# Kernel tuning notes

Hardware: AMD Instinct MI355X
Metric: run time of the kernel (lower is better)

## Reference

```python
import jax, jax.numpy as jnp
import numpy as np

N_NODES = 100000
N_EDGES = 600000
D_IN = 128
D_OUT = 512  # hidden_size * gates_num = 128 * 4


def setup_inputs() -> dict:
    key = jax.random.key(0)
    k1, k2, k3, k4 = jax.random.split(key, 4)
    x = jax.random.normal(k1, (N_NODES, D_IN), dtype=jnp.float32)
    edge_index = jax.random.randint(k2, (2, N_EDGES), 0, N_NODES, dtype=jnp.int64)
    W = jax.random.normal(k3, (D_OUT, D_IN), dtype=jnp.float32) * (1.0 / np.sqrt(D_IN))
    b = jax.random.normal(k4, (D_OUT,), dtype=jnp.float32) * 0.01
    return {"x": x, "edge_index": edge_index, "W": W, "b": b}


def reference(x, edge_index, W, b):
    row, col = edge_index[0], edge_index[1]
    # gather neighbor features and scatter-add into destination nodes
    agg = jax.ops.segment_sum(x[col], row, num_segments=x.shape[0])  # [N, D_IN]
    out = x + agg  # residual
    return out @ W.T + b  # [N, D_OUT]
```

## Files before the change

### kernel.cpp

```cpp
#include <hip/hip_runtime.h>
#include <hip/hip_bf16.h>

#define N_NODES 100000
#define N_EDGES 600000
#define D_IN 128
#define D_OUT 512
#define CAP 40
#define OVF_CAP 1024

typedef __bf16 bf16x8 __attribute__((ext_vector_type(8)));
typedef __bf16 bf16x2 __attribute__((ext_vector_type(2)));
typedef float f32x4 __attribute__((ext_vector_type(4)));

#define OFF_CNT   25600000
#define OFF_OVFC  26000000
#define OFF_OVF   26000016
#define OFF_BUCK  26008208

__global__ void k_bucket(const int* __restrict__ ei, int* __restrict__ cnt,
                         int* __restrict__ bucket, int* __restrict__ ovf_cnt,
                         int2* __restrict__ ovf) {
    int e = blockIdx.x * blockDim.x + threadIdx.x;
    if (e >= N_EDGES) return;
    int r = ei[e];
    int c = ei[N_EDGES + e];
    int slot = atomicAdd(&cnt[r], 1);
    if (slot < CAP) {
        bucket[(size_t)r * CAP + slot] = c;
    } else {
        int oi = atomicAdd(ovf_cnt, 1);
        if (oi < OVF_CAP) ovf[oi] = make_int2(r, c);
    }
}

__global__ void k_agg(const float* __restrict__ x, const int* __restrict__ cnt,
                      const int* __restrict__ bucket, const int* __restrict__ ovf_cnt,
                      const int2* __restrict__ ovf, __bf16* __restrict__ h) {
    int gw = (blockIdx.x * blockDim.x + threadIdx.x) >> 6;
    if (gw >= N_NODES) return;
    int lane = threadIdx.x & 63;
    const float2* xr = (const float2*)x;

    float2 acc = xr[(size_t)gw * 64 + lane];
    float ax2 = 0.f, ay2 = 0.f;

    int deg = __builtin_amdgcn_readfirstlane(cnt[gw]);
    int dmin = deg < CAP ? deg : CAP;
    const int* bk = bucket + (size_t)gw * CAP;

    int d = 0;
    for (; d + 1 < dmin; d += 2) {
        int c0 = __builtin_amdgcn_readfirstlane(bk[d]);
        int c1 = __builtin_amdgcn_readfirstlane(bk[d + 1]);
        float2 v0 = xr[(size_t)c0 * 64 + lane];
        float2 v1 = xr[(size_t)c1 * 64 + lane];
        acc.x += v0.x; acc.y += v0.y;
        ax2 += v1.x;   ay2 += v1.y;
    }
    if (d < dmin) {
        int c0 = __builtin_amdgcn_readfirstlane(bk[d]);
        float2 v0 = xr[(size_t)c0 * 64 + lane];
        acc.x += v0.x; acc.y += v0.y;
    }
    acc.x += ax2; acc.y += ay2;

    if (deg > CAP) {
        int n = *ovf_cnt;
        if (n > OVF_CAP) n = OVF_CAP;
        for (int i = 0; i < n; ++i) {
            int2 e = ovf[i];
            if (e.x == gw) {
                float2 v = xr[(size_t)e.y * 64 + lane];
                acc.x += v.x; acc.y += v.y;
            }
        }
    }

    bf16x2 o = { (__bf16)acc.x, (__bf16)acc.y };
    ((bf16x2*)h)[(size_t)gw * 64 + lane] = o;
}

#define BM 128
#define BN 64
#define LDA 136
#define LDB 136

__device__ inline bf16x8 cvt8(float4 v0, float4 v1) {
    bf16x8 u = { (__bf16)v0.x, (__bf16)v0.y, (__bf16)v0.z, (__bf16)v0.w,
                 (__bf16)v1.x, (__bf16)v1.y, (__bf16)v1.z, (__bf16)v1.w };
    return u;
}

__launch_bounds__(256, 2)
__global__ void k_gemm(const __bf16* __restrict__ h, const float* __restrict__ W,
                       const float* __restrict__ bias, float* __restrict__ out) {
    __shared__ __bf16 As[BM * LDA];
    __shared__ __bf16 Bs[BN * LDB];

    int tid = threadIdx.x;
    int m0 = blockIdx.y * BM;
    int n0 = blockIdx.x * BN;

    #pragma unroll
    for (int it = 0; it < 8; ++it) {
        int i = tid + it * 256;
        int r = i >> 4;
        int c = (i & 15) << 3;
        int gr = m0 + r;
        if (gr > N_NODES - 1) gr = N_NODES - 1;
        *(bf16x8*)&As[r * LDA + c] = *(const bf16x8*)(h + (size_t)gr * D_IN + c);
    }
    #pragma unroll
    for (int it = 0; it < 4; ++it) {
        int i = tid + it * 256;
        int r = i >> 4;
        int c = (i & 15) << 3;
        const float* src = W + (size_t)(n0 + r) * D_IN + c;
        float4 v0 = *(const float4*)(src);
        float4 v1 = *(const float4*)(src + 4);
        *(bf16x8*)&Bs[r * LDB + c] = cvt8(v0, v1);
    }
    __syncthreads();

    int lane = tid & 63;
    int wave = tid >> 6;
    int wm = wave & 1;
    int wn = wave >> 1;
    int quad = lane >> 4;
    int l16 = lane & 15;

    f32x4 acc[4][2] = {};

    const __bf16* Abase = &As[(wm * 64 + l16) * LDA + quad * 8];
    const __bf16* Bbase = &Bs[(wn * 32 + l16) * LDB + quad * 8];

    #pragma unroll
    for (int ks = 0; ks < 4; ++ks) {
        bf16x8 a0 = *(const bf16x8*)(Abase + ks * 32);
        bf16x8 a1 = *(const bf16x8*)(Abase + 16 * LDA + ks * 32);
        bf16x8 a2 = *(const bf16x8*)(Abase + 32 * LDA + ks * 32);
        bf16x8 a3 = *(const bf16x8*)(Abase + 48 * LDA + ks * 32);
        bf16x8 b0 = *(const bf16x8*)(Bbase + ks * 32);
        bf16x8 b1 = *(const bf16x8*)(Bbase + 16 * LDB + ks * 32);
        acc[0][0] = __builtin_amdgcn_mfma_f32_16x16x32_bf16(a0, b0, acc[0][0], 0, 0, 0);
        acc[0][1] = __builtin_amdgcn_mfma_f32_16x16x32_bf16(a0, b1, acc[0][1], 0, 0, 0);
        acc[1][0] = __builtin_amdgcn_mfma_f32_16x16x32_bf16(a1, b0, acc[1][0], 0, 0, 0);
        acc[1][1] = __builtin_amdgcn_mfma_f32_16x16x32_bf16(a1, b1, acc[1][1], 0, 0, 0);
        acc[2][0] = __builtin_amdgcn_mfma_f32_16x16x32_bf16(a2, b0, acc[2][0], 0, 0, 0);
        acc[2][1] = __builtin_amdgcn_mfma_f32_16x16x32_bf16(a2, b1, acc[2][1], 0, 0, 0);
        acc[3][0] = __builtin_amdgcn_mfma_f32_16x16x32_bf16(a3, b0, acc[3][0], 0, 0, 0);
        acc[3][1] = __builtin_amdgcn_mfma_f32_16x16x32_bf16(a3, b1, acc[3][1], 0, 0, 0);
    }

    float bias0 = bias[n0 + wn * 32 + l16];
    float bias1 = bias[n0 + wn * 32 + 16 + l16];
    #pragma unroll
    for (int mt = 0; mt < 4; ++mt) {
        int mrow = m0 + wm * 64 + mt * 16 + quad * 4;
        #pragma unroll
        for (int nt = 0; nt < 2; ++nt) {
            int ncol = n0 + wn * 32 + nt * 16 + l16;
            float bv = nt ? bias1 : bias0;
            #pragma unroll
            for (int rg = 0; rg < 4; ++rg) {
                int m = mrow + rg;
                if (m < N_NODES)
                    out[(size_t)m * D_OUT + ncol] = acc[mt][nt][rg] + bv;
            }
        }
    }
}

extern "C" void kernel_launch(void* const* d_in, const int* in_sizes, int n_in,
                              void* d_out, int out_size, void* d_ws, size_t ws_size,
                              hipStream_t stream) {
    const float* x  = (const float*)d_in[0];
    const int*   ei = (const int*)d_in[1];
    const float* W  = (const float*)d_in[2];
    const float* b  = (const float*)d_in[3];
    float* out = (float*)d_out;

    char* ws = (char*)d_ws;
    __bf16* h    = (__bf16*)ws;
    int* cnt     = (int*)(ws + OFF_CNT);
    int* ovf_cnt = (int*)(ws + OFF_OVFC);
    int2* ovf    = (int2*)(ws + OFF_OVF);
    int* bucket  = (int*)(ws + OFF_BUCK);

    hipMemsetAsync(cnt, 0, (OFF_OVFC - OFF_CNT) + 16, stream);

    k_bucket<<<(N_EDGES + 255) / 256, 256, 0, stream>>>(ei, cnt, bucket, ovf_cnt, ovf);
    k_agg<<<(N_NODES * 64 + 255) / 256, 256, 0, stream>>>(x, cnt, bucket, ovf_cnt, ovf, h);
    k_gemm<<<dim3(D_OUT / BN, (N_NODES + BM - 1) / BM), 256, 0, stream>>>(h, W, b, out);
}
```

Before: 389.7 us.

## Make GEMM persistent with register-resident W fragments and prefetched A strips

The GEMM becomes a persistent kernel: each wave holds a 128-column slice of W as bf16 MFMA fragments in registers and loops over 16-row strips of h. It loads the next strip directly from global memory while computing the current one, and drops shared memory and the block barrier. This removes the repeated per-block reloading and conversion of W and the LDS staging. The cost is heavy register use (128 VGPRs for the B fragments), which may limit occupancy under the 256-thread, 2-block launch bound, and only 512 concurrent waves stream the 100k-row output.

Result: slower. 403.7 us (+3.6%).

```diff
diff --git a/kernel.cpp b/kernel.cpp
--- a/kernel.cpp
+++ b/kernel.cpp
@@ -80,10 +80,9 @@
     ((bf16x2*)h)[(size_t)gw * 64 + lane] = o;
 }
 
-#define BM 128
-#define BN 64
-#define LDA 136
-#define LDB 136
+#define N_STRIPS 6250
+#define WAVE_SLOTS 512
+#define GEMM_ITERS 13
 
 __device__ inline bf16x8 cvt8(float4 v0, float4 v1) {
     bf16x8 u = { (__bf16)v0.x, (__bf16)v0.y, (__bf16)v0.z, (__bf16)v0.w,
@@ -94,80 +93,67 @@
 __launch_bounds__(256, 2)
 __global__ void k_gemm(const __bf16* __restrict__ h, const float* __restrict__ W,
                        const float* __restrict__ bias, float* __restrict__ out) {
-    __shared__ __bf16 As[BM * LDA];
-    __shared__ __bf16 Bs[BN * LDB];
-
     int tid = threadIdx.x;
-    int m0 = blockIdx.y * BM;
-    int n0 = blockIdx.x * BN;
-
-    #pragma unroll
-    for (int it = 0; it < 8; ++it) {
-        int i = tid + it * 256;
-        int r = i >> 4;
-        int c = (i & 15) << 3;
-        int gr = m0 + r;
-        if (gr > N_NODES - 1) gr = N_NODES - 1;
-        *(bf16x8*)&As[r * LDA + c] = *(const bf16x8*)(h + (size_t)gr * D_IN + c);
-    }
-    #pragma unroll
-    for (int it = 0; it < 4; ++it) {
-        int i = tid + it * 256;
-        int r = i >> 4;
-        int c = (i & 15) << 3;
-        const float* src = W + (size_t)(n0 + r) * D_IN + c;
-        float4 v0 = *(const float4*)(src);
-        float4 v1 = *(const float4*)(src + 4);
-        *(bf16x8*)&Bs[r * LDB + c] = cvt8(v0, v1);
-    }
-    __syncthreads();
-
     int lane = tid & 63;
     int wave = tid >> 6;
-    int wm = wave & 1;
-    int wn = wave >> 1;
-    int quad = lane >> 4;
-    int l16 = lane & 15;
+    int nq = blockIdx.x;
+    int q = lane >> 4;
+    int n16 = lane & 15;
 
-    f32x4 acc[4][2] = {};
+    bf16x8 bfrag[8][4];
+    {
+        const float* wb = W + (size_t)(nq * 128 + n16) * D_IN + q * 8;
+        #pragma unroll
+        for (int nt = 0; nt < 8; ++nt)
+            #pragma unroll
+            for (int ks = 0; ks < 4; ++ks) {
+                const float* src = wb + (size_t)nt * 16 * D_IN + ks * 32;
+                float4 v0 = *(const float4*)(src);
+                float4 v1 = *(const float4*)(src + 4);
+                bfrag[nt][ks] = cvt8(v0, v1);
+            }
+    }
+    float biasr[8];
+    #pragma unroll
+    for (int nt = 0; nt < 8; ++nt)
+        biasr[nt] = bias[nq * 128 + nt * 16 + n16];
 
-    const __bf16* Abase = &As[(wm * 64 + l16) * LDA + quad * 8];
-    const __bf16* Bbase = &Bs[(wn * 32 + l16) * LDB + quad * 8];
+    int g = blockIdx.y * 4 + wave;
 
-    #pragma unroll
-    for (int ks = 0; ks < 4; ++ks) {
-        bf16x8 a0 = *(const bf16x8*)(Abase + ks * 32);
-        bf16x8 a1 = *(const bf16x8*)(Abase + 16 * LDA + ks * 32);
-        bf16x8 a2 = *(const bf16x8*)(Abase + 32 * LDA + ks * 32);
-        bf16x8 a3 = *(const bf16x8*)(Abase + 48 * LDA + ks * 32);
-        bf16x8 b0 = *(const bf16x8*)(Bbase + ks * 32);
-        bf16x8 b1 = *(const bf16x8*)(Bbase + 16 * LDB + ks * 32);
-        acc[0][0] = __builtin_amdgcn_mfma_f32_16x16x32_bf16(a0, b0, acc[0][0], 0, 0, 0);
-        acc[0][1] = __builtin_amdgcn_mfma_f32_16x16x32_bf16(a0, b1, acc[0][1], 0, 0, 0);
-        acc[1][0] = __builtin_amdgcn_mfma_f32_16x16x32_bf16(a1, b0, acc[1][0], 0, 0, 0);
-        acc[1][1] = __builtin_amdgcn_mfma_f32_16x16x32_bf16(a1, b1, acc[1][1], 0, 0, 0);
-        acc[2][0] = __builtin_amdgcn_mfma_f32_16x16x32_bf16(a2, b0, acc[2][0], 0, 0, 0);
-        acc[2][1] = __builtin_amdgcn_mfma_f32_16x16x32_bf16(a2, b1, acc[2][1], 0, 0, 0);
-        acc[3][0] = __builtin_amdgcn_mfma_f32_16x16x32_bf16(a3, b0, acc[3][0], 0, 0, 0);
-        acc[3][1] = __builtin_amdgcn_mfma_f32_16x16x32_bf16(a3, b1, acc[3][1], 0, 0, 0);
+    bf16x8 af[4];
+    if (g < N_STRIPS) {
+        const __bf16* ab = h + (size_t)(g * 16 + n16) * D_IN + q * 8;
+        #pragma unroll
+        for (int ks = 0; ks < 4; ++ks) af[ks] = *(const bf16x8*)(ab + ks * 32);
     }
 
-    float bias0 = bias[n0 + wn * 32 + l16];
-    float bias1 = bias[n0 + wn * 32 + 16 + l16];
-    #pragma unroll
-    for (int mt = 0; mt < 4; ++mt) {
-        int mrow = m0 + wm * 64 + mt * 16 + quad * 4;
-        #pragma unroll
-        for (int nt = 0; nt < 2; ++nt) {
-            int ncol = n0 + wn * 32 + nt * 16 + l16;
-            float bv = nt ? bias1 : bias0;
+    for (int it = 0; it < GEMM_ITERS; ++it) {
+        int gn = g + WAVE_SLOTS;
+        bf16x8 afn[4];
+        if (it + 1 < GEMM_ITERS && gn < N_STRIPS) {
+            const __bf16* ab = h + (size_t)(gn * 16 + n16) * D_IN + q * 8;
             #pragma unroll
-            for (int rg = 0; rg < 4; ++rg) {
-                int m = mrow + rg;
-                if (m < N_NODES)
-                    out[(size_t)m * D_OUT + ncol] = acc[mt][nt][rg] + bv;
+            for (int ks = 0; ks < 4; ++ks) afn[ks] = *(const bf16x8*)(ab + ks * 32);
+        }
+        if (g < N_STRIPS) {
+            f32x4 acc[8] = {};
+            #pragma unroll
+            for (int ks = 0; ks < 4; ++ks)
+                #pragma unroll
+                for (int nt = 0; nt < 8; ++nt)
+                    acc[nt] = __builtin_amdgcn_mfma_f32_16x16x32_bf16(
+                        af[ks], bfrag[nt][ks], acc[nt], 0, 0, 0);
+            float* ob = out + (size_t)(g * 16 + q * 4) * D_OUT + nq * 128 + n16;
+            #pragma unroll
+            for (int nt = 0; nt < 8; ++nt) {
+                #pragma unroll
+                for (int rg = 0; rg < 4; ++rg)
+                    ob[(size_t)rg * D_OUT + nt * 16] = acc[nt][rg] + biasr[nt];
             }
         }
+        g = gn;
+        #pragma unroll
+        for (int ks = 0; ks < 4; ++ks) af[ks] = afn[ks];
     }
 }
 
@@ -191,5 +177,5 @@
 
     k_bucket<<<(N_EDGES + 255) / 256, 256, 0, stream>>>(ei, cnt, bucket, ovf_cnt, ovf);
     k_agg<<<(N_NODES * 64 + 255) / 256, 256, 0, stream>>>(x, cnt, bucket, ovf_cnt, ovf, h);
-    k_gemm<<<dim3(D_OUT / BN, (N_NODES + BM - 1) / BM), 256, 0, stream>>>(h, W, b, out);
+    k_gemm<<<dim3(4, 128), 256, 0, stream>>>(h, W, b, out);
 }
```
